# Kernel tuning notes

Measured on AMD Instinct MI355X. Metric: run time of the kernel, lower is better.

The kernel has to match this reference:

```python
import jax, jax.numpy as jnp
import numpy as np

# Forest of complete binary trees modeling query plans.
B = 512          # number of plans (trees)
D = 11           # tree depth; leaves at level D-1
LEAVES = 1 << (D - 1)      # 1024 leaves per tree
N_INT = LEAVES - 1         # 1023 internal nodes per tree (BFS heap order)
F_LEAF = 64      # leaf ('Scan') feature dim
F_INT = 32       # internal operator feature dim
H = 128          # hidden_dim
NHID = 4         # num_layers=5 -> input layer + 4 hidden layers
DV = 32          # data_vec_dim
OUT = 1 + DV     # latency + data vector


def _mlp(x, W_in, b_in, W_hid, b_hid, W_out, b_out):
    """GenericUnit: Linear+ReLU input layer, NHID Linear+ReLU hidden layers, linear output."""
    h = jax.nn.relu(x @ W_in + b_in)
    for i in range(W_hid.shape[0]):  # small fixed loop over layers
        h = jax.nn.relu(h @ W_hid[i] + b_hid[i])
    return h @ W_out + b_out


def setup_inputs() -> dict:
    key = jax.random.key(0)
    ks = jax.random.split(key, 8)

    def w(k, shape, fan_in):
        return jax.random.normal(k, shape, jnp.float32) * np.float32(1.0 / np.sqrt(fan_in))

    return {
        "leaf_feat": jax.random.normal(ks[0], (B, LEAVES, F_LEAF), jnp.float32),
        "int_feat": jax.random.normal(ks[1], (B, N_INT, F_INT), jnp.float32),
        # leaf unit (0 children)
        "leaf_W_in": w(ks[2], (F_LEAF, H), F_LEAF),
        "leaf_b_in": jnp.zeros((H,), jnp.float32),
        "leaf_W_hid": w(ks[3], (NHID, H, H), H),
        "leaf_b_hid": jnp.zeros((NHID, H), jnp.float32),
        "leaf_W_out": w(ks[4], (H, OUT), H),
        "leaf_b_out": jnp.zeros((OUT,), jnp.float32),
        # internal unit (2 children): input = F_INT + 2*OUT = 98
        "int_W_in": w(ks[5], (F_INT + 2 * OUT, H), F_INT + 2 * OUT),
        "int_b_in": jnp.zeros((H,), jnp.float32),
        "int_W_hid": w(ks[6], (NHID, H, H), H),
        "int_b_hid": jnp.zeros((NHID, H), jnp.float32),
        "int_W_out": w(ks[7], (H, OUT), H),
        "int_b_out": jnp.zeros((OUT,), jnp.float32),
    }


def reference(leaf_feat, int_feat,
              leaf_W_in, leaf_b_in, leaf_W_hid, leaf_b_hid, leaf_W_out, leaf_b_out,
              int_W_in, int_b_in, int_W_hid, int_b_hid, int_W_out, int_b_out):
    # Leaves (level D-1): [B, LEAVES, OUT]
    cur = _mlp(leaf_feat, leaf_W_in, leaf_b_in, leaf_W_hid, leaf_b_hid, leaf_W_out, leaf_b_out)
    # Bottom-up over internal levels; level d has 2^d nodes at BFS offsets [2^d-1, 2^(d+1)-1)
    for d in range(D - 2, -1, -1):
        n = 1 << d
        feats = int_feat[:, n - 1: 2 * n - 1, :]            # [B, n, F_INT]
        children = cur.reshape(B, n, 2 * OUT)               # concat of two child outputs
        unit_in = jnp.concatenate([feats, children], axis=-1)
        cur = _mlp(unit_in, int_W_in, int_b_in, int_W_hid, int_b_hid, int_W_out, int_b_out)
    # Root output, latency channel: [B]
    return cur[:, 0, 0]
```

## Files before the change

### kernel.cpp

```cpp
#include <hip/hip_runtime.h>
#include <cstdint>
#include <cstddef>

constexpr int Bn     = 512;
constexpr int Dd     = 11;
constexpr int LEAVES = 1024;
constexpr int NINT   = 1023;
constexpr int FLEAF  = 64;
constexpr int FINT   = 32;
constexpr int Hh     = 128;
constexpr int NHIDl  = 4;
constexpr int OUTC   = 33;
constexpr int KINT   = FINT + 2 * OUTC;

#define THREADS 256
constexpr int M_TILE = 64;
constexpr int KSTR   = 136;
constexpr int MATSZ  = 128 * KSTR;

using short8 = __attribute__((ext_vector_type(8))) short;
using f32x4  = __attribute__((ext_vector_type(4))) float;

__device__ __forceinline__ unsigned short f2bf(float f) {
  unsigned int u = __float_as_uint(f);
  u += 0x7fff + ((u >> 16) & 1);
  return (unsigned short)(u >> 16);
}
__device__ __forceinline__ float bf2f(unsigned short h) {
  return __uint_as_float(((unsigned int)h) << 16);
}

template <int KCHUNKS>
__device__ __forceinline__ void dense_layer_mfma(
    unsigned short* Ah, unsigned short* Al,
    const unsigned short* __restrict__ WTh, const unsigned short* __restrict__ WTl,
    const float* __restrict__ bias)
{
  const int tid  = threadIdx.x;
  const int wave = tid >> 6;
  const int lane = tid & 63;
  const int quad = lane >> 4;
  const int l16  = lane & 15;
  const int nbase = wave * 32;

  f32x4 c[4][2];
#pragma unroll
  for (int mt = 0; mt < 4; ++mt)
#pragma unroll
    for (int nt = 0; nt < 2; ++nt) c[mt][nt] = (f32x4){0.f, 0.f, 0.f, 0.f};

#pragma unroll
  for (int kc = 0; kc < KCHUNKS; ++kc) {
    const int k0 = kc * 32 + quad * 8;
    short8 a_h[4], a_l[4];
#pragma unroll
    for (int mt = 0; mt < 4; ++mt) {
      const int row = mt * 16 + l16;
      a_h[mt] = *(const short8*)&Ah[row * KSTR + k0];
      a_l[mt] = *(const short8*)&Al[row * KSTR + k0];
    }
    short8 b_h[2], b_l[2];
#pragma unroll
    for (int nt = 0; nt < 2; ++nt) {
      const int n = nbase + nt * 16 + l16;
      b_h[nt] = *(const short8*)&WTh[n * KSTR + k0];
      b_l[nt] = *(const short8*)&WTl[n * KSTR + k0];
    }
#pragma unroll
    for (int nt = 0; nt < 2; ++nt)
#pragma unroll
      for (int mt = 0; mt < 4; ++mt) {
        c[mt][nt] = __builtin_amdgcn_mfma_f32_16x16x32_bf16(a_h[mt], b_h[nt], c[mt][nt], 0, 0, 0);
        c[mt][nt] = __builtin_amdgcn_mfma_f32_16x16x32_bf16(a_l[mt], b_h[nt], c[mt][nt], 0, 0, 0);
        c[mt][nt] = __builtin_amdgcn_mfma_f32_16x16x32_bf16(a_h[mt], b_l[nt], c[mt][nt], 0, 0, 0);
      }
  }
  __syncthreads();

#pragma unroll
  for (int nt = 0; nt < 2; ++nt) {
    const int n = nbase + nt * 16 + l16;
    const float bv = bias[n];
#pragma unroll
    for (int mt = 0; mt < 4; ++mt)
#pragma unroll
      for (int r = 0; r < 4; ++r) {
        const int row = mt * 16 + quad * 4 + r;
        float v = c[mt][nt][r] + bv;
        v = fmaxf(v, 0.f);
        const unsigned short h = f2bf(v);
        const unsigned short lo = f2bf(v - bf2f(h));
        Ah[row * KSTR + n] = h;
        Al[row * KSTR + n] = lo;
      }
  }
  __syncthreads();
}

__device__ __forceinline__ void out_layer_mfma(
    const unsigned short* Ah, const unsigned short* Al,
    const unsigned short* __restrict__ WTh, const unsigned short* __restrict__ WTl,
    const float* __restrict__ bias, float* __restrict__ outg, int row_base)
{
  const int tid  = threadIdx.x;
  const int wave = tid >> 6;
  const int lane = tid & 63;
  const int quad = lane >> 4;
  const int l16  = lane & 15;
  if (wave >= 3) return;

  f32x4 c[4];
#pragma unroll
  for (int mt = 0; mt < 4; ++mt) c[mt] = (f32x4){0.f, 0.f, 0.f, 0.f};

#pragma unroll
  for (int kc = 0; kc < 4; ++kc) {
    const int k0 = kc * 32 + quad * 8;
    const int n  = wave * 16 + l16;
    const short8 b_h = *(const short8*)&WTh[n * KSTR + k0];
    const short8 b_l = *(const short8*)&WTl[n * KSTR + k0];
#pragma unroll
    for (int mt = 0; mt < 4; ++mt) {
      const int row = mt * 16 + l16;
      const short8 a_h = *(const short8*)&Ah[row * KSTR + k0];
      const short8 a_l = *(const short8*)&Al[row * KSTR + k0];
      c[mt] = __builtin_amdgcn_mfma_f32_16x16x32_bf16(a_h, b_h, c[mt], 0, 0, 0);
      c[mt] = __builtin_amdgcn_mfma_f32_16x16x32_bf16(a_l, b_h, c[mt], 0, 0, 0);
      c[mt] = __builtin_amdgcn_mfma_f32_16x16x32_bf16(a_h, b_l, c[mt], 0, 0, 0);
    }
  }

  const int n = wave * 16 + l16;
  if (n < OUTC) {
    const float bv = bias[n];
#pragma unroll
    for (int mt = 0; mt < 4; ++mt)
#pragma unroll
      for (int r = 0; r < 4; ++r) {
        const int row = mt * 16 + quad * 4 + r;
        outg[(size_t)(row_base + row) * OUTC + n] = c[mt][r] + bv;
      }
  }
}

__global__ __launch_bounds__(THREADS, 2)
void leaf_kernel(const float* __restrict__ X,
                 const unsigned short* __restrict__ warena,
                 const float* __restrict__ barena,
                 float* __restrict__ out)
{
  __shared__ unsigned short Ah[M_TILE * KSTR];
  __shared__ unsigned short Al[M_TILE * KSTR];
  const int row_base = blockIdx.x * M_TILE;
  const int tid = threadIdx.x;

  for (int e = tid; e < M_TILE * (FLEAF / 4); e += THREADS) {
    const int r  = e >> 4;
    const int k0 = (e & 15) << 2;
    const float4 v = *(const float4*)&X[(size_t)(row_base + r) * FLEAF + k0];
    const float vv[4] = {v.x, v.y, v.z, v.w};
    unsigned short hs[4], ls[4];
#pragma unroll
    for (int j = 0; j < 4; ++j) {
      hs[j] = f2bf(vv[j]);
      ls[j] = f2bf(vv[j] - bf2f(hs[j]));
    }
    *(ushort4*)&Ah[r * KSTR + k0] = *(ushort4*)hs;
    *(ushort4*)&Al[r * KSTR + k0] = *(ushort4*)ls;
  }
  __syncthreads();

  dense_layer_mfma<2>(Ah, Al, warena + 0 * 2 * MATSZ, warena + 0 * 2 * MATSZ + MATSZ, barena + 0 * 128);
#pragma unroll
  for (int l = 0; l < NHIDl; ++l) {
    const int id = 1 + l;
    dense_layer_mfma<4>(Ah, Al, warena + id * 2 * MATSZ, warena + id * 2 * MATSZ + MATSZ, barena + id * 128);
  }
  out_layer_mfma(Ah, Al, warena + 5 * 2 * MATSZ, warena + 5 * 2 * MATSZ + MATSZ, barena + 5 * 128, out, row_base);
}

__global__ __launch_bounds__(THREADS, 2)
void int_kernel(const float* __restrict__ feat, const float* __restrict__ prev,
                const unsigned short* __restrict__ warena,
                const float* __restrict__ barena,
                float* __restrict__ out, int n, int logn)
{
  __shared__ unsigned short Ah[M_TILE * KSTR];
  __shared__ unsigned short Al[M_TILE * KSTR];
  const int row_base = blockIdx.x * M_TILE;
  const int tid = threadIdx.x;

  for (int e = tid; e < M_TILE * KINT; e += THREADS) {
    const int m = e / KINT;
    const int k = e - m * KINT;
    const int row = row_base + m;
    const int b = row >> logn;
    const int i = row & (n - 1);
    float v;
    if (k < FINT) {
      v = feat[((size_t)b * NINT + (n - 1) + i) * FINT + k];
    } else {
      v = prev[((size_t)b * (n << 1) + (i << 1)) * OUTC + (k - FINT)];
    }
    const unsigned short h = f2bf(v);
    Ah[m * KSTR + k] = h;
    Al[m * KSTR + k] = f2bf(v - bf2f(h));
  }
  for (int e = tid; e < M_TILE * (Hh - KINT); e += THREADS) {
    const int m = e / (Hh - KINT);
    const int k = KINT + (e - m * (Hh - KINT));
    Ah[m * KSTR + k] = 0;
    Al[m * KSTR + k] = 0;
  }
  __syncthreads();

  dense_layer_mfma<4>(Ah, Al, warena + 6 * 2 * MATSZ, warena + 6 * 2 * MATSZ + MATSZ, barena + 6 * 128);
#pragma unroll
  for (int l = 0; l < NHIDl; ++l) {
    const int id = 7 + l;
    dense_layer_mfma<4>(Ah, Al, warena + id * 2 * MATSZ, warena + id * 2 * MATSZ + MATSZ, barena + id * 128);
  }
  out_layer_mfma(Ah, Al, warena + 11 * 2 * MATSZ, warena + 11 * 2 * MATSZ + MATSZ, barena + 11 * 128, out, row_base);
}

__global__ void prep_kernel(const float* __restrict__ lW_in, const float* __restrict__ lW_hid,
                            const float* __restrict__ lW_out, const float* __restrict__ lb_in,
                            const float* __restrict__ lb_hid, const float* __restrict__ lb_out,
                            const float* __restrict__ iW_in, const float* __restrict__ iW_hid,
                            const float* __restrict__ iW_out, const float* __restrict__ ib_in,
                            const float* __restrict__ ib_hid, const float* __restrict__ ib_out,
                            unsigned short* __restrict__ warena, float* __restrict__ barena)
{
  const int id = blockIdx.y;
  const float* W; const float* bsrc; int K, N;
  if (id == 0)       { W = lW_in;                     bsrc = lb_in;               K = FLEAF; N = Hh; }
  else if (id <= 4)  { W = lW_hid + (id - 1) * Hh*Hh; bsrc = lb_hid + (id-1)*Hh;  K = Hh;    N = Hh; }
  else if (id == 5)  { W = lW_out;                    bsrc = lb_out;              K = Hh;    N = OUTC; }
  else if (id == 6)  { W = iW_in;                     bsrc = ib_in;               K = KINT;  N = Hh; }
  else if (id <= 10) { W = iW_hid + (id - 7) * Hh*Hh; bsrc = ib_hid + (id-7)*Hh;  K = Hh;    N = Hh; }
  else               { W = iW_out;                    bsrc = ib_out;              K = Hh;    N = OUTC; }

  unsigned short* dsth = warena + id * 2 * MATSZ;
  unsigned short* dstl = dsth + MATSZ;

  const int e = blockIdx.x * THREADS + threadIdx.x;
  if (e < MATSZ) {
    const int nn = e / KSTR;
    const int kp = e - nn * KSTR;
    float val = 0.f;
    if (kp < K && nn < N) val = W[(size_t)kp * N + nn];
    const unsigned short h = f2bf(val);
    dsth[e] = h;
    dstl[e] = f2bf(val - bf2f(h));
  }
  if (blockIdx.x == 0 && threadIdx.x < 128) {
    const int t = threadIdx.x;
    barena[id * 128 + t] = (t < N) ? bsrc[t] : 0.f;
  }
}

__global__ void gather_kernel(const float* __restrict__ buf, float* __restrict__ out) {
  const int b = blockIdx.x * blockDim.x + threadIdx.x;
  if (b < Bn) out[b] = buf[(size_t)b * OUTC];
}

extern "C" void kernel_launch(void* const* d_in, const int* in_sizes, int n_in,
                              void* d_out, int out_size, void* d_ws, size_t ws_size,
                              hipStream_t stream) {
  const float* leaf_feat = (const float*)d_in[0];
  const float* int_feat  = (const float*)d_in[1];
  const float* lW_in  = (const float*)d_in[2];
  const float* lb_in  = (const float*)d_in[3];
  const float* lW_hid = (const float*)d_in[4];
  const float* lb_hid = (const float*)d_in[5];
  const float* lW_out = (const float*)d_in[6];
  const float* lb_out = (const float*)d_in[7];
  const float* iW_in  = (const float*)d_in[8];
  const float* ib_in  = (const float*)d_in[9];
  const float* iW_hid = (const float*)d_in[10];
  const float* ib_hid = (const float*)d_in[11];
  const float* iW_out = (const float*)d_in[12];
  const float* ib_out = (const float*)d_in[13];
  float* out = (float*)d_out;

  float* bufA = (float*)d_ws;
  float* bufB = bufA + (size_t)Bn * LEAVES * OUTC;
  unsigned short* warena = (unsigned short*)(bufB + (size_t)Bn * (LEAVES / 2) * OUTC);
  float* barena = (float*)(warena + 24 * MATSZ);

  prep_kernel<<<dim3((MATSZ + THREADS - 1) / THREADS, 12), THREADS, 0, stream>>>(
      lW_in, lW_hid, lW_out, lb_in, lb_hid, lb_out,
      iW_in, iW_hid, iW_out, ib_in, ib_hid, ib_out, warena, barena);

  leaf_kernel<<<(Bn * LEAVES) / M_TILE, THREADS, 0, stream>>>(leaf_feat, warena, barena, bufA);

  float* prev = bufA;
  float* next = bufB;
  for (int d = Dd - 2; d >= 0; --d) {
    const int n = 1 << d;
    const int blocks = (Bn * n) / M_TILE;
    int_kernel<<<blocks, THREADS, 0, stream>>>(int_feat, prev, warena, barena, next, n, d);
    float* t = prev; prev = next; next = t;
  }

  gather_kernel<<<1, Bn, 0, stream>>>(prev, out);
}
```

Before: 1.020 ms.

## Store activations as bf16 hi/lo pairs, hoist weights, fuse small tree levels into one kernel

Intermediate child outputs are now stored in global memory as split bf16 hi/lo arrays instead of fp32, so the next level copies them straight into shared memory without conversion. Weight hi fragments and biases are loaded into registers once per layer. Epilogue packing is vectorized, using truncation for the hi half and RNE for the lo half. The six smallest levels (32 nodes down to the root) run in one per-tree tail kernel that keeps results in shared memory, which removes several tiny launches and the gather kernel. Launch bounds rise to 4 blocks per CU. The main risk is register pressure from the hoisted weights at that occupancy target.

```diff
diff --git a/kernel.cpp b/kernel.cpp
--- a/kernel.cpp
+++ b/kernel.cpp
@@ -9,29 +9,38 @@
 constexpr int FLEAF  = 64;
 constexpr int FINT   = 32;
 constexpr int Hh     = 128;
-constexpr int NHIDl  = 4;
 constexpr int OUTC   = 33;
-constexpr int KINT   = FINT + 2 * OUTC;
 
 #define THREADS 256
-constexpr int M_TILE = 64;
-constexpr int KSTR   = 136;
-constexpr int MATSZ  = 128 * KSTR;
+constexpr int KSTR  = 136;
+constexpr int MATSZ = 128 * KSTR;
 
 using short8 = __attribute__((ext_vector_type(8))) short;
 using f32x4  = __attribute__((ext_vector_type(4))) float;
 
-__device__ __forceinline__ unsigned short f2bf(float f) {
+__device__ __forceinline__ unsigned int f2bf_rne_u(float f) {
   unsigned int u = __float_as_uint(f);
-  u += 0x7fff + ((u >> 16) & 1);
-  return (unsigned short)(u >> 16);
+  u += 0x7fffu + ((u >> 16) & 1);
+  return u;
+}
+__device__ __forceinline__ unsigned short f2bf_rne(float f) {
+  return (unsigned short)(f2bf_rne_u(f) >> 16);
 }
 __device__ __forceinline__ float bf2f(unsigned short h) {
-  return __uint_as_float(((unsigned int)h) << 16);
-}
-
-template <int KCHUNKS>
-__device__ __forceinline__ void dense_layer_mfma(
+  return __uint_as_float((unsigned int)h << 16);
+}
+__device__ __forceinline__ float trunc_bf(float a) {
+  return __uint_as_float(__float_as_uint(a) & 0xffff0000u);
+}
+__device__ __forceinline__ unsigned int pack_hi_trunc(float a, float b) {
+  return (__float_as_uint(a) >> 16) | (__float_as_uint(b) & 0xffff0000u);
+}
+__device__ __forceinline__ unsigned int pack_lo_rne(float a, float b) {
+  return (f2bf_rne_u(a) >> 16) | (f2bf_rne_u(b) & 0xffff0000u);
+}
+
+template <int KC, int MT>
+__device__ __forceinline__ void dense_layer(
     unsigned short* Ah, unsigned short* Al,
     const unsigned short* __restrict__ WTh, const unsigned short* __restrict__ WTl,
     const float* __restrict__ bias)
@@ -43,184 +52,296 @@
   const int l16  = lane & 15;
   const int nbase = wave * 32;
 
-  f32x4 c[4][2];
-#pragma unroll
-  for (int mt = 0; mt < 4; ++mt)
+  short8 wh[2][KC];
+#pragma unroll
+  for (int nt = 0; nt < 2; ++nt) {
+    const int n = nbase + nt * 16 + l16;
+#pragma unroll
+    for (int kc = 0; kc < KC; ++kc)
+      wh[nt][kc] = *(const short8*)&WTh[n * KSTR + kc * 32 + quad * 8];
+  }
+  float4 bv[2];
+#pragma unroll
+  for (int nt = 0; nt < 2; ++nt)
+    bv[nt] = *(const float4*)&bias[nbase + nt * 16 + quad * 4];
+
+  f32x4 c[MT][2];
+#pragma unroll
+  for (int mt = 0; mt < MT; ++mt)
 #pragma unroll
     for (int nt = 0; nt < 2; ++nt) c[mt][nt] = (f32x4){0.f, 0.f, 0.f, 0.f};
 
 #pragma unroll
-  for (int kc = 0; kc < KCHUNKS; ++kc) {
+  for (int kc = 0; kc < KC; ++kc) {
     const int k0 = kc * 32 + quad * 8;
-    short8 a_h[4], a_l[4];
-#pragma unroll
-    for (int mt = 0; mt < 4; ++mt) {
-      const int row = mt * 16 + l16;
-      a_h[mt] = *(const short8*)&Ah[row * KSTR + k0];
-      a_l[mt] = *(const short8*)&Al[row * KSTR + k0];
-    }
-    short8 b_h[2], b_l[2];
+    short8 wl[2];
 #pragma unroll
     for (int nt = 0; nt < 2; ++nt) {
       const int n = nbase + nt * 16 + l16;
-      b_h[nt] = *(const short8*)&WTh[n * KSTR + k0];
-      b_l[nt] = *(const short8*)&WTl[n * KSTR + k0];
-    }
-#pragma unroll
-    for (int nt = 0; nt < 2; ++nt)
-#pragma unroll
-      for (int mt = 0; mt < 4; ++mt) {
-        c[mt][nt] = __builtin_amdgcn_mfma_f32_16x16x32_bf16(a_h[mt], b_h[nt], c[mt][nt], 0, 0, 0);
-        c[mt][nt] = __builtin_amdgcn_mfma_f32_16x16x32_bf16(a_l[mt], b_h[nt], c[mt][nt], 0, 0, 0);
-        c[mt][nt] = __builtin_amdgcn_mfma_f32_16x16x32_bf16(a_h[mt], b_l[nt], c[mt][nt], 0, 0, 0);
-      }
+      wl[nt] = *(const short8*)&WTl[n * KSTR + k0];
+    }
+    short8 ah[MT], al[MT];
+#pragma unroll
+    for (int mt = 0; mt < MT; ++mt) {
+      ah[mt] = *(const short8*)&Ah[(mt * 16 + l16) * KSTR + k0];
+      al[mt] = *(const short8*)&Al[(mt * 16 + l16) * KSTR + k0];
+    }
+#pragma unroll
+    for (int mt = 0; mt < MT; ++mt)
+#pragma unroll
+      for (int nt = 0; nt < 2; ++nt)
+        c[mt][nt] = __builtin_amdgcn_mfma_f32_16x16x32_bf16(wh[nt][kc], ah[mt], c[mt][nt], 0, 0, 0);
+#pragma unroll
+    for (int mt = 0; mt < MT; ++mt)
+#pragma unroll
+      for (int nt = 0; nt < 2; ++nt)
+        c[mt][nt] = __builtin_amdgcn_mfma_f32_16x16x32_bf16(wh[nt][kc], al[mt], c[mt][nt], 0, 0, 0);
+#pragma unroll
+    for (int mt = 0; mt < MT; ++mt)
+#pragma unroll
+      for (int nt = 0; nt < 2; ++nt)
+        c[mt][nt] = __builtin_amdgcn_mfma_f32_16x16x32_bf16(wl[nt], ah[mt], c[mt][nt], 0, 0, 0);
   }
   __syncthreads();
 
 #pragma unroll
-  for (int nt = 0; nt < 2; ++nt) {
-    const int n = nbase + nt * 16 + l16;
-    const float bv = bias[n];
-#pragma unroll
-    for (int mt = 0; mt < 4; ++mt)
-#pragma unroll
-      for (int r = 0; r < 4; ++r) {
-        const int row = mt * 16 + quad * 4 + r;
-        float v = c[mt][nt][r] + bv;
-        v = fmaxf(v, 0.f);
-        const unsigned short h = f2bf(v);
-        const unsigned short lo = f2bf(v - bf2f(h));
-        Ah[row * KSTR + n] = h;
-        Al[row * KSTR + n] = lo;
-      }
+  for (int mt = 0; mt < MT; ++mt) {
+    const int m = mt * 16 + l16;
+#pragma unroll
+    for (int nt = 0; nt < 2; ++nt) {
+      const int nb = nbase + nt * 16 + quad * 4;
+      float v0 = fmaxf(c[mt][nt][0] + bv[nt].x, 0.f);
+      float v1 = fmaxf(c[mt][nt][1] + bv[nt].y, 0.f);
+      float v2 = fmaxf(c[mt][nt][2] + bv[nt].z, 0.f);
+      float v3 = fmaxf(c[mt][nt][3] + bv[nt].w, 0.f);
+      const unsigned int h0 = pack_hi_trunc(v0, v1);
+      const unsigned int h1 = pack_hi_trunc(v2, v3);
+      const unsigned int l0 = pack_lo_rne(v0 - trunc_bf(v0), v1 - trunc_bf(v1));
+      const unsigned int l1 = pack_lo_rne(v2 - trunc_bf(v2), v3 - trunc_bf(v3));
+      *(uint2*)&Ah[m * KSTR + nb] = make_uint2(h0, h1);
+      *(uint2*)&Al[m * KSTR + nb] = make_uint2(l0, l1);
+    }
   }
   __syncthreads();
 }
 
-__device__ __forceinline__ void out_layer_mfma(
+template <int MT>
+__device__ __forceinline__ void out_layer(
     const unsigned short* Ah, const unsigned short* Al,
     const unsigned short* __restrict__ WTh, const unsigned short* __restrict__ WTl,
-    const float* __restrict__ bias, float* __restrict__ outg, int row_base)
+    const float* __restrict__ bias,
+    unsigned short* outH, unsigned short* outL, float* finalOut)
 {
   const int tid  = threadIdx.x;
   const int wave = tid >> 6;
   const int lane = tid & 63;
   const int quad = lane >> 4;
   const int l16  = lane & 15;
-  if (wave >= 3) return;
-
-  f32x4 c[4];
-#pragma unroll
-  for (int mt = 0; mt < 4; ++mt) c[mt] = (f32x4){0.f, 0.f, 0.f, 0.f};
-
-#pragma unroll
-  for (int kc = 0; kc < 4; ++kc) {
-    const int k0 = kc * 32 + quad * 8;
-    const int n  = wave * 16 + l16;
-    const short8 b_h = *(const short8*)&WTh[n * KSTR + k0];
-    const short8 b_l = *(const short8*)&WTl[n * KSTR + k0];
-#pragma unroll
-    for (int mt = 0; mt < 4; ++mt) {
-      const int row = mt * 16 + l16;
-      const short8 a_h = *(const short8*)&Ah[row * KSTR + k0];
-      const short8 a_l = *(const short8*)&Al[row * KSTR + k0];
-      c[mt] = __builtin_amdgcn_mfma_f32_16x16x32_bf16(a_h, b_h, c[mt], 0, 0, 0);
-      c[mt] = __builtin_amdgcn_mfma_f32_16x16x32_bf16(a_l, b_h, c[mt], 0, 0, 0);
-      c[mt] = __builtin_amdgcn_mfma_f32_16x16x32_bf16(a_h, b_l, c[mt], 0, 0, 0);
-    }
-  }
-
-  const int n = wave * 16 + l16;
-  if (n < OUTC) {
-    const float bv = bias[n];
-#pragma unroll
-    for (int mt = 0; mt < 4; ++mt)
+  if (wave < 3) {
+    const int n_row = wave * 16 + l16;
+    short8 wh[4], wl[4];
+#pragma unroll
+    for (int kc = 0; kc < 4; ++kc) {
+      wh[kc] = *(const short8*)&WTh[n_row * KSTR + kc * 32 + quad * 8];
+      wl[kc] = *(const short8*)&WTl[n_row * KSTR + kc * 32 + quad * 8];
+    }
+    const int nb = wave * 16 + quad * 4;
+    const float4 bv = *(const float4*)&bias[nb];
+    const float bvr[4] = {bv.x, bv.y, bv.z, bv.w};
+
+    f32x4 c[MT];
+#pragma unroll
+    for (int mt = 0; mt < MT; ++mt) c[mt] = (f32x4){0.f, 0.f, 0.f, 0.f};
+#pragma unroll
+    for (int kc = 0; kc < 4; ++kc) {
+      const int k0 = kc * 32 + quad * 8;
+#pragma unroll
+      for (int mt = 0; mt < MT; ++mt) {
+        const short8 ah = *(const short8*)&Ah[(mt * 16 + l16) * KSTR + k0];
+        const short8 al = *(const short8*)&Al[(mt * 16 + l16) * KSTR + k0];
+        c[mt] = __builtin_amdgcn_mfma_f32_16x16x32_bf16(wh[kc], ah, c[mt], 0, 0, 0);
+        c[mt] = __builtin_amdgcn_mfma_f32_16x16x32_bf16(wh[kc], al, c[mt], 0, 0, 0);
+        c[mt] = __builtin_amdgcn_mfma_f32_16x16x32_bf16(wl[kc], ah, c[mt], 0, 0, 0);
+      }
+    }
+#pragma unroll
+    for (int mt = 0; mt < MT; ++mt) {
+      const int m = mt * 16 + l16;
 #pragma unroll
       for (int r = 0; r < 4; ++r) {
-        const int row = mt * 16 + quad * 4 + r;
-        outg[(size_t)(row_base + row) * OUTC + n] = c[mt][r] + bv;
-      }
-  }
-}
-
-__global__ __launch_bounds__(THREADS, 2)
+        const int n = nb + r;
+        const float v = c[mt][r] + bvr[r];
+        if (n < OUTC) {
+          outH[m * 33 + n] = (unsigned short)(__float_as_uint(v) >> 16);
+          outL[m * 33 + n] = f2bf_rne(v - trunc_bf(v));
+        }
+        if (finalOut && n == 0 && m == 0) *finalOut = v;
+      }
+    }
+  }
+}
+
+__global__ __launch_bounds__(THREADS, 4)
 void leaf_kernel(const float* __restrict__ X,
                  const unsigned short* __restrict__ warena,
                  const float* __restrict__ barena,
-                 float* __restrict__ out)
-{
-  __shared__ unsigned short Ah[M_TILE * KSTR];
-  __shared__ unsigned short Al[M_TILE * KSTR];
-  const int row_base = blockIdx.x * M_TILE;
+                 unsigned short* __restrict__ outH, unsigned short* __restrict__ outL)
+{
+  __shared__ unsigned short Ah[64 * KSTR];
+  __shared__ unsigned short Al[64 * KSTR];
+  const int row_base = blockIdx.x * 64;
   const int tid = threadIdx.x;
 
-  for (int e = tid; e < M_TILE * (FLEAF / 4); e += THREADS) {
+  for (int e = tid; e < 64 * 16; e += THREADS) {
     const int r  = e >> 4;
     const int k0 = (e & 15) << 2;
     const float4 v = *(const float4*)&X[(size_t)(row_base + r) * FLEAF + k0];
-    const float vv[4] = {v.x, v.y, v.z, v.w};
-    unsigned short hs[4], ls[4];
+    const unsigned int h0 = pack_hi_trunc(v.x, v.y);
+    const unsigned int h1 = pack_hi_trunc(v.z, v.w);
+    const unsigned int l0 = pack_lo_rne(v.x - trunc_bf(v.x), v.y - trunc_bf(v.y));
+    const unsigned int l1 = pack_lo_rne(v.z - trunc_bf(v.z), v.w - trunc_bf(v.w));
+    *(uint2*)&Ah[r * KSTR + k0] = make_uint2(h0, h1);
+    *(uint2*)&Al[r * KSTR + k0] = make_uint2(l0, l1);
+  }
+  __syncthreads();
+
+  dense_layer<2, 4>(Ah, Al, warena + 0 * 2 * MATSZ, warena + 0 * 2 * MATSZ + MATSZ, barena + 0 * 128);
+#pragma unroll
+  for (int l = 0; l < 4; ++l) {
+    const int id = 1 + l;
+    dense_layer<4, 4>(Ah, Al, warena + id * 2 * MATSZ, warena + id * 2 * MATSZ + MATSZ, barena + id * 128);
+  }
+  out_layer<4>(Ah, Al, warena + 5 * 2 * MATSZ, warena + 5 * 2 * MATSZ + MATSZ, barena + 5 * 128,
+               outH + (size_t)row_base * 33, outL + (size_t)row_base * 33, nullptr);
+}
+
+__global__ __launch_bounds__(THREADS, 4)
+void int_kernel(const float* __restrict__ feat,
+                const unsigned short* __restrict__ prevH, const unsigned short* __restrict__ prevL,
+                const unsigned short* __restrict__ warena, const float* __restrict__ barena,
+                unsigned short* __restrict__ outH, unsigned short* __restrict__ outL,
+                int n, int logn)
+{
+  __shared__ unsigned short Ah[64 * KSTR];
+  __shared__ unsigned short Al[64 * KSTR];
+  const int tid = threadIdx.x;
+  const int m = tid & 63;
+  const int g = tid >> 6;
+  const int row = blockIdx.x * 64 + m;
+  const int b = row >> logn;
+  const int i = row & (n - 1);
+
+  const float* fr = feat + ((size_t)b * NINT + (n - 1) + i) * FINT;
+#pragma unroll
+  for (int j = 0; j < 4; ++j) {
+    const int cch = g + 4 * j;
+    const float2 v = *(const float2*)&fr[cch * 2];
+    *(unsigned int*)&Ah[m * KSTR + cch * 2] = pack_hi_trunc(v.x, v.y);
+    *(unsigned int*)&Al[m * KSTR + cch * 2] = pack_lo_rne(v.x - trunc_bf(v.x), v.y - trunc_bf(v.y));
+  }
+  const size_t c0 = ((size_t)b * (n << 1) + (i << 1)) * 33;
+#pragma unroll
+  for (int j = 0; j < 9; ++j) {
+    const int p = g + 4 * j;
+    if (p < 33) {
+      const unsigned int hv = *(const unsigned int*)&prevH[c0 + 2 * p];
+      const unsigned int lv = *(const unsigned int*)&prevL[c0 + 2 * p];
+      *(unsigned int*)&Ah[m * KSTR + 32 + 2 * p] = hv;
+      *(unsigned int*)&Al[m * KSTR + 32 + 2 * p] = lv;
+    }
+  }
+#pragma unroll
+  for (int j = 0; j < 4; ++j) {
+    const int p = g + 4 * j;
+    if (p < 15) {
+      *(unsigned int*)&Ah[m * KSTR + 98 + 2 * p] = 0u;
+      *(unsigned int*)&Al[m * KSTR + 98 + 2 * p] = 0u;
+    }
+  }
+  __syncthreads();
+
+  dense_layer<4, 4>(Ah, Al, warena + 6 * 2 * MATSZ, warena + 6 * 2 * MATSZ + MATSZ, barena + 6 * 128);
+#pragma unroll
+  for (int l = 0; l < 4; ++l) {
+    const int id = 7 + l;
+    dense_layer<4, 4>(Ah, Al, warena + id * 2 * MATSZ, warena + id * 2 * MATSZ + MATSZ, barena + id * 128);
+  }
+  out_layer<4>(Ah, Al, warena + 11 * 2 * MATSZ, warena + 11 * 2 * MATSZ + MATSZ, barena + 11 * 128,
+               outH + (size_t)blockIdx.x * 64 * 33, outL + (size_t)blockIdx.x * 64 * 33, nullptr);
+}
+
+__global__ __launch_bounds__(THREADS, 4)
+void tail_kernel(const float* __restrict__ feat,
+                 const unsigned short* __restrict__ g6H, const unsigned short* __restrict__ g6L,
+                 const unsigned short* __restrict__ warena, const float* __restrict__ barena,
+                 float* __restrict__ out)
+{
+  __shared__ unsigned short Ah[64 * KSTR];
+  __shared__ unsigned short Al[64 * KSTR];
+  __shared__ unsigned short oH[64 * 33];
+  __shared__ unsigned short oL[64 * 33];
+  const int tid = threadIdx.x;
+  const int m = tid & 63;
+  const int g = tid >> 6;
+  const int b = blockIdx.x;
+
+  for (int d = 5; d >= 0; --d) {
+    const int n = 1 << d;
+    const int i = m & (n - 1);
+    const float* fr = feat + ((size_t)b * NINT + (n - 1) + i) * FINT;
 #pragma unroll
     for (int j = 0; j < 4; ++j) {
-      hs[j] = f2bf(vv[j]);
-      ls[j] = f2bf(vv[j] - bf2f(hs[j]));
-    }
-    *(ushort4*)&Ah[r * KSTR + k0] = *(ushort4*)hs;
-    *(ushort4*)&Al[r * KSTR + k0] = *(ushort4*)ls;
-  }
-  __syncthreads();
-
-  dense_layer_mfma<2>(Ah, Al, warena + 0 * 2 * MATSZ, warena + 0 * 2 * MATSZ + MATSZ, barena + 0 * 128);
-#pragma unroll
-  for (int l = 0; l < NHIDl; ++l) {
-    const int id = 1 + l;
-    dense_layer_mfma<4>(Ah, Al, warena + id * 2 * MATSZ, warena + id * 2 * MATSZ + MATSZ, barena + id * 128);
-  }
-  out_layer_mfma(Ah, Al, warena + 5 * 2 * MATSZ, warena + 5 * 2 * MATSZ + MATSZ, barena + 5 * 128, out, row_base);
-}
-
-__global__ __launch_bounds__(THREADS, 2)
-void int_kernel(const float* __restrict__ feat, const float* __restrict__ prev,
-                const unsigned short* __restrict__ warena,
-                const float* __restrict__ barena,
-                float* __restrict__ out, int n, int logn)
-{
-  __shared__ unsigned short Ah[M_TILE * KSTR];
-  __shared__ unsigned short Al[M_TILE * KSTR];
-  const int row_base = blockIdx.x * M_TILE;
-  const int tid = threadIdx.x;
-
-  for (int e = tid; e < M_TILE * KINT; e += THREADS) {
-    const int m = e / KINT;
-    const int k = e - m * KINT;
-    const int row = row_base + m;
-    const int b = row >> logn;
-    const int i = row & (n - 1);
-    float v;
-    if (k < FINT) {
-      v = feat[((size_t)b * NINT + (n - 1) + i) * FINT + k];
+      const int cch = g + 4 * j;
+      const float2 v = *(const float2*)&fr[cch * 2];
+      *(unsigned int*)&Ah[m * KSTR + cch * 2] = pack_hi_trunc(v.x, v.y);
+      *(unsigned int*)&Al[m * KSTR + cch * 2] = pack_lo_rne(v.x - trunc_bf(v.x), v.y - trunc_bf(v.y));
+    }
+    const unsigned short* sH;
+    const unsigned short* sL;
+    size_t c0;
+    if (d == 5) { sH = g6H; sL = g6L; c0 = ((size_t)b * 64 + 2 * i) * 33; }
+    else        { sH = oH;  sL = oL;  c0 = (size_t)(2 * i) * 33; }
+#pragma unroll
+    for (int j = 0; j < 9; ++j) {
+      const int p = g + 4 * j;
+      if (p < 33) {
+        const unsigned int hv = *(const unsigned int*)&sH[c0 + 2 * p];
+        const unsigned int lv = *(const unsigned int*)&sL[c0 + 2 * p];
+        *(unsigned int*)&Ah[m * KSTR + 32 + 2 * p] = hv;
+        *(unsigned int*)&Al[m * KSTR + 32 + 2 * p] = lv;
+      }
+    }
+#pragma unroll
+    for (int j = 0; j < 4; ++j) {
+      const int p = g + 4 * j;
+      if (p < 15) {
+        *(unsigned int*)&Ah[m * KSTR + 98 + 2 * p] = 0u;
+        *(unsigned int*)&Al[m * KSTR + 98 + 2 * p] = 0u;
+      }
+    }
+    __syncthreads();
+
+    if (d == 5) {
+      dense_layer<4, 2>(Ah, Al, warena + 6 * 2 * MATSZ, warena + 6 * 2 * MATSZ + MATSZ, barena + 6 * 128);
+#pragma unroll
+      for (int l = 0; l < 4; ++l) {
+        const int id = 7 + l;
+        dense_layer<4, 2>(Ah, Al, warena + id * 2 * MATSZ, warena + id * 2 * MATSZ + MATSZ, barena + id * 128);
+      }
+      out_layer<2>(Ah, Al, warena + 11 * 2 * MATSZ, warena + 11 * 2 * MATSZ + MATSZ, barena + 11 * 128,
+                   oH, oL, nullptr);
     } else {
-      v = prev[((size_t)b * (n << 1) + (i << 1)) * OUTC + (k - FINT)];
-    }
-    const unsigned short h = f2bf(v);
-    Ah[m * KSTR + k] = h;
-    Al[m * KSTR + k] = f2bf(v - bf2f(h));
-  }
-  for (int e = tid; e < M_TILE * (Hh - KINT); e += THREADS) {
-    const int m = e / (Hh - KINT);
-    const int k = KINT + (e - m * (Hh - KINT));
-    Ah[m * KSTR + k] = 0;
-    Al[m * KSTR + k] = 0;
-  }
-  __syncthreads();
-
-  dense_layer_mfma<4>(Ah, Al, warena + 6 * 2 * MATSZ, warena + 6 * 2 * MATSZ + MATSZ, barena + 6 * 128);
-#pragma unroll
-  for (int l = 0; l < NHIDl; ++l) {
-    const int id = 7 + l;
-    dense_layer_mfma<4>(Ah, Al, warena + id * 2 * MATSZ, warena + id * 2 * MATSZ + MATSZ, barena + id * 128);
-  }
-  out_layer_mfma(Ah, Al, warena + 11 * 2 * MATSZ, warena + 11 * 2 * MATSZ + MATSZ, barena + 11 * 128, out, row_base);
+      dense_layer<4, 1>(Ah, Al, warena + 6 * 2 * MATSZ, warena + 6 * 2 * MATSZ + MATSZ, barena + 6 * 128);
+#pragma unroll
+      for (int l = 0; l < 4; ++l) {
+        const int id = 7 + l;
+        dense_layer<4, 1>(Ah, Al, warena + id * 2 * MATSZ, warena + id * 2 * MATSZ + MATSZ, barena + id * 128);
+      }
+      out_layer<1>(Ah, Al, warena + 11 * 2 * MATSZ, warena + 11 * 2 * MATSZ + MATSZ, barena + 11 * 128,
+                   oH, oL, (d == 0) ? (out + b) : nullptr);
+    }
+    __syncthreads();
+  }
 }
 
 __global__ void prep_kernel(const float* __restrict__ lW_in, const float* __restrict__ lW_hid,
@@ -232,36 +353,27 @@
                             unsigned short* __restrict__ warena, float* __restrict__ barena)
 {
   const int id = blockIdx.y;
-  const float* W; const float* bsrc; int K, N;
-  if (id == 0)       { W = lW_in;                     bsrc = lb_in;               K = FLEAF; N = Hh; }
-  else if (id <= 4)  { W = lW_hid + (id - 1) * Hh*Hh; bsrc = lb_hid + (id-1)*Hh;  K = Hh;    N = Hh; }
-  else if (id == 5)  { W = lW_out;                    bsrc = lb_out;              K = Hh;    N = OUTC; }
-  else if (id == 6)  { W = iW_in;                     bsrc = ib_in;               K = KINT;  N = Hh; }
-  else if (id <= 10) { W = iW_hid + (id - 7) * Hh*Hh; bsrc = ib_hid + (id-7)*Hh;  K = Hh;    N = Hh; }
-  else               { W = iW_out;                    bsrc = ib_out;              K = Hh;    N = OUTC; }
-
-  unsigned short* dsth = warena + id * 2 * MATSZ;
-  unsigned short* dstl = dsth + MATSZ;
-
+  const float* W; const float* bs; int K, N;
+  if (id == 0)       { W = lW_in;                        bs = lb_in;                 K = FLEAF; N = Hh; }
+  else if (id <= 4)  { W = lW_hid + (id - 1) * Hh * Hh;  bs = lb_hid + (id - 1) * Hh; K = Hh;   N = Hh; }
+  else if (id == 5)  { W = lW_out;                       bs = lb_out;                K = Hh;    N = OUTC; }
+  else if (id == 6)  { W = iW_in;                        bs = ib_in;                 K = FINT + 2 * OUTC; N = Hh; }
+  else if (id <= 10) { W = iW_hid + (id - 7) * Hh * Hh;  bs = ib_hid + (id - 7) * Hh; K = Hh;   N = Hh; }
+  else               { W = iW_out;                       bs = ib_out;                K = Hh;    N = OUTC; }
+
+  unsigned short* dh = warena + id * 2 * MATSZ;
+  unsigned short* dl = dh + MATSZ;
   const int e = blockIdx.x * THREADS + threadIdx.x;
   if (e < MATSZ) {
     const int nn = e / KSTR;
-    const int kp = e - nn * KSTR;
-    float val = 0.f;
-    if (kp < K && nn < N) val = W[(size_t)kp * N + nn];
-    const unsigned short h = f2bf(val);
-    dsth[e] = h;
-    dstl[e] = f2bf(val - bf2f(h));
-  }
-  if (blockIdx.x == 0 && threadIdx.x < 128) {
-    const int t = threadIdx.x;
-    barena[id * 128 + t] = (t < N) ? bsrc[t] : 0.f;
-  }
-}
-
-__global__ void gather_kernel(const float* __restrict__ buf, float* __restrict__ out) {
-  const int b = blockIdx.x * blockDim.x + threadIdx.x;
-  if (b < Bn) out[b] = buf[(size_t)b * OUTC];
+    const int kk = e - nn * KSTR;
+    const float v = (kk < K && nn < N) ? W[(size_t)kk * N + nn] : 0.f;
+    const unsigned short h = f2bf_rne(v);
+    dh[e] = h;
+    dl[e] = f2bf_rne(v - bf2f(h));
+  }
+  if (blockIdx.x == 0 && threadIdx.x < 128)
+    barena[id * 128 + threadIdx.x] = (threadIdx.x < N) ? bs[threadIdx.x] : 0.f;
 }
 
 extern "C" void kernel_launch(void* const* d_in, const int* in_sizes, int n_in,
@@ -283,25 +395,25 @@
   const float* ib_out = (const float*)d_in[13];
   float* out = (float*)d_out;
 
-  float* bufA = (float*)d_ws;
-  float* bufB = bufA + (size_t)Bn * LEAVES * OUTC;
-  unsigned short* warena = (unsigned short*)(bufB + (size_t)Bn * (LEAVES / 2) * OUTC);
+  const size_t rowsA = (size_t)Bn * LEAVES;
+  const size_t rowsB = rowsA / 2;
+  unsigned short* AH = (unsigned short*)d_ws;
+  unsigned short* AL = AH + rowsA * 33;
+  unsigned short* BH = AL + rowsA * 33;
+  unsigned short* BL = BH + rowsB * 33;
+  unsigned short* warena = BL + rowsB * 33;
   float* barena = (float*)(warena + 24 * MATSZ);
 
   prep_kernel<<<dim3((MATSZ + THREADS - 1) / THREADS, 12), THREADS, 0, stream>>>(
       lW_in, lW_hid, lW_out, lb_in, lb_hid, lb_out,
       iW_in, iW_hid, iW_out, ib_in, ib_hid, ib_out, warena, barena);
 
-  leaf_kernel<<<(Bn * LEAVES) / M_TILE, THREADS, 0, stream>>>(leaf_feat, warena, barena, bufA);
-
-  float* prev = bufA;
-  float* next = bufB;
-  for (int d = Dd - 2; d >= 0; --d) {
-    const int n = 1 << d;
-    const int blocks = (Bn * n) / M_TILE;
-    int_kernel<<<blocks, THREADS, 0, stream>>>(int_feat, prev, warena, barena, next, n, d);
-    float* t = prev; prev = next; next = t;
-  }
-
-  gather_kernel<<<1, Bn, 0, stream>>>(prev, out);
-}
+  leaf_kernel<<<(Bn * LEAVES) / 64, THREADS, 0, stream>>>(leaf_feat, warena, barena, AH, AL);
+
+  int_kernel<<<4096, THREADS, 0, stream>>>(int_feat, AH, AL, warena, barena, BH, BL, 512, 9);
+  int_kernel<<<2048, THREADS, 0, stream>>>(int_feat, BH, BL, warena, barena, AH, AL, 256, 8);
+  int_kernel<<<1024, THREADS, 0, stream>>>(int_feat, AH, AL, warena, barena, BH, BL, 128, 7);
+  int_kernel<<< 512, THREADS, 0, stream>>>(int_feat, BH, BL, warena, barena, AH, AL,  64, 6);
+
+  tail_kernel<<<Bn, THREADS, 0, stream>>>(int_feat, AH, AL, warena, barena, out);
+}
```

After: 913.7 us. -10.4%, faster.
